# Kernel tuning notes

Measured on AMD Instinct MI355X. Metric: run time of the kernel, lower is better.

The kernel has to match this reference:

```python
import jax, jax.numpy as jnp
import numpy as np

NUM_SUBSET = 3
BN_EPS = 1e-5
T_CONST = 40
NUM_HEADS = 8


def _unit_gcn(x, PA, Wa, ba, Wb, bb, Wd, bd, gamma, beta):
    # x: (B, C, T, V). 1x1 convs become channel einsums. flag=True, GMPool_G,
    # num_point not in {3,7} -> adjacency A = PA only. down = identity (C_in==C_out).
    B, C, T, V = x.shape
    inter = Wa.shape[1]
    x_flat = x.reshape(B, C * T, V)
    y = None
    for i in range(NUM_SUBSET):
        a = jnp.einsum('bctv,ic->bitv', x, Wa[i]) + ba[i][None, :, None, None]
        A1 = a.transpose(0, 3, 1, 2).reshape(B, V, inter * T)          # (B, V, inter*T)
        b = jnp.einsum('bctv,ic->bitv', x, Wb[i]) + bb[i][None, :, None, None]
        A2 = b.reshape(B, inter * T, V)                                 # (B, inter*T, V)
        S = jax.nn.softmax((A1 @ A2) / (inter * T), axis=-2) + PA[i]    # (B, V, V), Softmax(-2)
        z = (x_flat @ S).reshape(B, C, T, V)
        z = jnp.einsum('bctv,oc->botv', z, Wd[i]) + bd[i][None, :, None, None]
        y = z if y is None else y + z
    # BatchNorm2d (eval: running_mean=0, running_var=1)
    y = y * (gamma / jnp.sqrt(1.0 + BN_EPS))[None, :, None, None] + beta[None, :, None, None]
    y = y + x  # residual via identity down-path
    return jax.nn.relu(y)


def _mab_forward(Q, K, fck, fcv, fco):
    B, Npt, DK = K.shape
    T = T_CONST
    C = DK // T
    Kr = K.transpose(0, 2, 1).reshape(B, C, T, Npt)   # (B, C, T, V)
    Kg = _unit_gcn(Kr, *fck)
    Vg = _unit_gcn(Kr, *fcv)
    Kf = Kg.transpose(0, 3, 1, 2).reshape(B, Npt, -1)  # (B, V, C*T)
    Vf = Vg.transpose(0, 3, 1, 2).reshape(B, Npt, -1)
    S, DV = Q.shape[1], Q.shape[2]
    ds = DV // NUM_HEADS
    Qh = Q.reshape(B, S, NUM_HEADS, ds)
    Kh = Kf.reshape(B, Npt, NUM_HEADS, ds)
    Vh = Vf.reshape(B, Npt, NUM_HEADS, ds)
    scores = jnp.einsum('bqhd,bkhd->bhqk', Qh, Kh) / jnp.sqrt(jnp.float32(DV))
    attn = jax.nn.softmax(scores, axis=-1)  # softmax_dim=2 of (H*B, S, V) == last axis
    Oh = Qh + jnp.einsum('bhqk,bkhd->bqhd', attn, Vh)
    O = Oh.reshape(B, S, DV)  # cat over heads along feature dim == reshape
    Og = O.transpose(0, 2, 1).reshape(B, C, T, S)
    Og = _unit_gcn(Og, *fco)
    Og = Og.transpose(0, 3, 1, 2).reshape(B, S, -1)
    return O + jax.nn.relu(Og)


def setup_inputs() -> dict:
    key = jax.random.key(0)
    ks = jax.random.split(key, 8)
    B, Npt, Sd, T, C, inter = 256, 25, 10, 40, 64, 16
    D = C * T  # 2560

    def gcn_params(kk, V):
        k = jax.random.split(kk, 5)
        return dict(
            PA=jnp.full((3, V, V), 1e-6, jnp.float32),
            Wa=jax.random.normal(k[0], (3, inter, C), jnp.float32) * np.float32(np.sqrt(2.0 / C)),
            ba=jnp.zeros((3, inter), jnp.float32),
            Wb=jax.random.normal(k[1], (3, inter, C), jnp.float32) * np.float32(np.sqrt(2.0 / C)),
            bb=jnp.zeros((3, inter), jnp.float32),
            Wd=jax.random.normal(k[2], (3, C, C), jnp.float32) * np.float32(np.sqrt(2.0 / (3 * C))),
            bd=jnp.zeros((3, C), jnp.float32),
            gamma=jax.random.uniform(k[3], (C,), jnp.float32, 0.5, 1.5),
            beta=jax.random.normal(k[4], (C,), jnp.float32) * 0.01,
        )

    inp = {
        'Q': jax.random.normal(ks[0], (B, Sd, D), jnp.float32),
        'K': jax.random.normal(ks[1], (B, Npt, D), jnp.float32),
    }
    for pref, kk, V in (('fck', ks[2], Npt), ('fcv', ks[3], Npt), ('fco', ks[4], Sd)):
        for n, v in gcn_params(kk, V).items():
            inp[pref + '_' + n] = v
    for n in ('relrec_s1', 'relsend_s1', 'relrec_s2', 'relsend_s2', 'relrec_speed', 'relsend_speed'):
        inp[n] = jnp.zeros((1,), jnp.int32)  # unused (branch only active for V==7, T==20)
    return inp


def reference(Q, K,
              fck_PA, fck_Wa, fck_ba, fck_Wb, fck_bb, fck_Wd, fck_bd, fck_gamma, fck_beta,
              fcv_PA, fcv_Wa, fcv_ba, fcv_Wb, fcv_bb, fcv_Wd, fcv_bd, fcv_gamma, fcv_beta,
              fco_PA, fco_Wa, fco_ba, fco_Wb, fco_bb, fco_Wd, fco_bd, fco_gamma, fco_beta,
              relrec_s1, relsend_s1, relrec_s2, relsend_s2, relrec_speed, relsend_speed):
    fck = (fck_PA, fck_Wa, fck_ba, fck_Wb, fck_bb, fck_Wd, fck_bd, fck_gamma, fck_beta)
    fcv = (fcv_PA, fcv_Wa, fcv_ba, fcv_Wb, fcv_bb, fcv_Wd, fcv_bd, fcv_gamma, fcv_beta)
    fco = (fco_PA, fco_Wa, fco_ba, fco_Wb, fco_bb, fco_Wd, fco_bd, fco_gamma, fco_beta)
    return _mab_forward(Q, K, fck, fcv, fco)
```

## Files before the change

kernel.cpp:

```cpp
#include <hip/hip_runtime.h>
#include <hip/hip_bf16.h>

#define BB 256
#define CC 64
#define TT 40
#define DD 2560
#define V1 25
#define V2 10
#define INTER 16
#define NH 8
#define DSH 320
#define HSLAB 8000

typedef __hip_bfloat16 bf16;
typedef unsigned int uint;
typedef unsigned short ushort;
typedef __attribute__((ext_vector_type(8))) short bf16x8;
typedef __attribute__((ext_vector_type(4))) float f32x4;

__device__ __forceinline__ float b2f(bf16 x) { return __bfloat162float(x); }

__device__ __forceinline__ ushort f2bb(float f) {
    uint x = __float_as_uint(f);
    uint r = x + 0x7fffu + ((x >> 16) & 1u);
    return (ushort)(r >> 16);
}
__device__ __forceinline__ float blo(uint u) { return __uint_as_float(u << 16); }
__device__ __forceinline__ float bhi(uint u) { return __uint_as_float(u & 0xffff0000u); }
__device__ __forceinline__ float b2f_us(ushort h) { return __uint_as_float(((uint)h) << 16); }
__device__ __forceinline__ uint4 pack8(const float* a) {
    uint4 pk;
    pk.x = (uint)f2bb(a[0]) | ((uint)f2bb(a[1]) << 16);
    pk.y = (uint)f2bb(a[2]) | ((uint)f2bb(a[3]) << 16);
    pk.z = (uint)f2bb(a[4]) | ((uint)f2bb(a[5]) << 16);
    pk.w = (uint)f2bb(a[6]) | ((uint)f2bb(a[7]) << 16);
    return pk;
}

__device__ __forceinline__ int swz64(int row, int col) {
    return row * 64 + ((((col >> 3) ^ row) & 7) << 3) + (col & 7);
}
__device__ __forceinline__ int swzC(int c, int col) {
    return c * 128 + ((((col >> 3) ^ c) & 15) << 3) + (col & 7);
}

__global__ __launch_bounds__(256) void gcn_S3(
    const float* __restrict__ X,
    const float* __restrict__ Wa0, const float* __restrict__ ba0,
    const float* __restrict__ Wb0, const float* __restrict__ bb0,
    const float* __restrict__ Wa1, const float* __restrict__ ba1,
    const float* __restrict__ Wb1, const float* __restrict__ bb1,
    bf16* __restrict__ Xw, float* __restrict__ Mpart) {
    __shared__ ushort xsT[208][72];
    __shared__ ushort wT[64][72];
    __shared__ ushort abT[4][32][136];
    __shared__ float biasS[64];

    const int tid = threadIdx.x;
    const int b = blockIdx.x & 255, tc = blockIdx.x >> 8;
    const int t0 = tc * 8;
    const int lane = tid & 63, w = tid >> 6;
    const int ln = lane & 15, lq = lane >> 4;

    const float* Xb = X + (size_t)b * V1 * DD;
    for (int e = tid; e < V1 * 64; e += 256) {
        const int v = e >> 6, c = e & 63;
        const float* src = Xb + (size_t)v * DD + c * TT + t0;
        const float4 f0 = *(const float4*)src;
        const float4 f1 = *(const float4*)(src + 4);
        const float tmp[8] = {f0.x, f0.y, f0.z, f0.w, f1.x, f1.y, f1.z, f1.w};
        #pragma unroll
        for (int tl = 0; tl < 8; ++tl) xsT[v * 8 + tl][c] = f2bb(tmp[tl]);
    }
    __syncthreads();

    for (int e = tid; e < 1600; e += 256) {
        const int v = e >> 6, h = (e >> 3) & 7, tl = e & 7;
        *(uint4*)(Xw + (size_t)(b * NH + h) * HSLAB + v * 320 + (t0 + tl) * 8) =
            *(const uint4*)&xsT[v * 8 + tl][h * 8];
    }

    for (int s = 0; s < 3; ++s) {
        if (s) __syncthreads();
        for (int e = tid; e < 4096; e += 256) {
            const int mat = e >> 10, r = e & 1023;
            const float* Wp = (mat == 0) ? Wa0 : (mat == 1) ? Wb0 : (mat == 2) ? Wa1 : Wb1;
            wT[(mat << 4) + (r >> 6)][r & 63] = f2bb(Wp[s * 1024 + r]);
        }
        if (tid < 64) {
            const int mat = tid >> 4, j = tid & 15;
            const float* bp = (mat == 0) ? ba0 : (mat == 1) ? bb0 : (mat == 2) ? ba1 : bb1;
            biasS[tid] = bp[s * 16 + j];
        }
        __syncthreads();

        const bf16x8 a0 = *(const bf16x8*)&wT[w * 16 + ln][lq * 8];
        const bf16x8 a1 = *(const bf16x8*)&wT[w * 16 + ln][lq * 8 + 32];
        float br[4];
        #pragma unroll
        for (int r = 0; r < 4; ++r) br[r] = biasS[w * 16 + lq * 4 + r];
        for (int nt = 0; nt < 13; ++nt) {
            const bf16x8 b0 = *(const bf16x8*)&xsT[nt * 16 + ln][lq * 8];
            const bf16x8 b1 = *(const bf16x8*)&xsT[nt * 16 + ln][lq * 8 + 32];
            f32x4 acc = (f32x4){0.f, 0.f, 0.f, 0.f};
            acc = __builtin_amdgcn_mfma_f32_16x16x32_bf16(a0, b0, acc, 0, 0, 0);
            acc = __builtin_amdgcn_mfma_f32_16x16x32_bf16(a1, b1, acc, 0, 0, 0);
            const int p = nt * 16 + ln;
            if (p < 200) {
                const int v = p >> 3, tl = p & 7;
                #pragma unroll
                for (int r = 0; r < 4; ++r)
                    abT[w][v][(lq * 4 + r) * 8 + tl] = f2bb(acc[r] + br[r]);
            }
        }
        __syncthreads();

        #pragma unroll
        for (int uu = 0; uu < 2; ++uu) {
            const int u = w + uu * 4;
            const int np = u >> 2, mt = (u >> 1) & 1, ntl = u & 1;
            const ushort* Ap = &abT[np * 2 + 0][mt * 16 + ln][lq * 8];
            const ushort* Bp = &abT[np * 2 + 1][ntl * 16 + ln][lq * 8];
            f32x4 g = (f32x4){0.f, 0.f, 0.f, 0.f};
            g = __builtin_amdgcn_mfma_f32_16x16x32_bf16(
                    *(const bf16x8*)Ap, *(const bf16x8*)Bp, g, 0, 0, 0);
            g = __builtin_amdgcn_mfma_f32_16x16x32_bf16(
                    *(const bf16x8*)(Ap + 32), *(const bf16x8*)(Bp + 32), g, 0, 0, 0);
            g = __builtin_amdgcn_mfma_f32_16x16x32_bf16(
                    *(const bf16x8*)(Ap + 64), *(const bf16x8*)(Bp + 64), g, 0, 0, 0);
            g = __builtin_amdgcn_mfma_f32_16x16x32_bf16(
                    *(const bf16x8*)(Ap + 96), *(const bf16x8*)(Bp + 96), g, 0, 0, 0);
            const int vp = ntl * 16 + ln;
            if (vp < V1) {
                float* Mb = Mpart + (((size_t)tc * 256 + b) * 6 + (s * 2 + np)) * 625;
                #pragma unroll
                for (int r = 0; r < 4; ++r) {
                    const int v = mt * 16 + lq * 4 + r;
                    if (v < V1) Mb[v * V1 + vp] = g[r];
                }
            }
        }
    }
}

__global__ __launch_bounds__(128) void reduce_softmax(
    const float* __restrict__ Mpart,
    const float* __restrict__ PA0, const float* __restrict__ PA1,
    const float* __restrict__ WdK, const float* __restrict__ WdV,
    ushort* __restrict__ Sbf, ushort* __restrict__ Wdf) {
    __shared__ float Ms[625];
    const int tid = threadIdx.x, b = blockIdx.x, snp = blockIdx.y;
    const int s = snp >> 1, np = snp & 1;

    if (b == 0) {
        for (int e = tid; e < 256; e += 128) {
            const int wv = e >> 6, l = e & 63;
            const int lnn = l & 15, lqq = l >> 4;
            const float* Wp = (np ? WdV : WdK) + s * 4096 + (wv * 16 + lnn) * 64 + lqq * 8;
            ushort* dst = Wdf + (((np * 3 + s) * 4 + wv) * 64 + l) * 16;
            #pragma unroll
            for (int j = 0; j < 8; ++j) {
                dst[j] = f2bb(Wp[j]);
                dst[8 + j] = f2bb(Wp[32 + j]);
            }
        }
    }

    for (int e = tid; e < 625; e += 128) {
        float sum = 0.f;
        #pragma unroll
        for (int tcc = 0; tcc < 5; ++tcc)
            sum += Mpart[(((size_t)tcc * 256 + b) * 6 + snp) * 625 + e];
        Ms[e] = sum;
    }
    __syncthreads();
    if (tid < 32) {
        ushort* SbfRow = Sbf + ((((size_t)b * 2 + np) * 3 + s) << 10) + tid * 32;
        if (tid < V1) {
            const int vp = tid;
            const float invIT = 1.0f / 640.0f;
            float mx = -1e30f;
            for (int v = 0; v < V1; ++v) mx = fmaxf(mx, Ms[v * V1 + vp]);
            float sum = 0.f;
            for (int v = 0; v < V1; ++v) sum += expf((Ms[v * V1 + vp] - mx) * invIT);
            const float rs = 1.f / sum;
            const float* PAn = np ? PA1 : PA0;
            for (int v = 0; v < V1; ++v) {
                const float e_ = expf((Ms[v * V1 + vp] - mx) * invIT);
                SbfRow[v] = f2bb(e_ * rs + PAn[(s * V1 + v) * V1 + vp]);
            }
            for (int v = V1; v < 32; ++v) SbfRow[v] = 0;
        } else {
            for (int v = 0; v < 32; ++v) SbfRow[v] = 0;
        }
    }
}

__global__ __launch_bounds__(256) void gcn_S2O(
    const float* __restrict__ X,
    const float* __restrict__ Wa0, const float* __restrict__ ba0,
    const float* __restrict__ Wb0, const float* __restrict__ bb0,
    const float* __restrict__ PA0, const float* __restrict__ WdO,
    ushort* __restrict__ SbfO, ushort* __restrict__ Wdf3) {
    constexpr int V = V2;
    constexpr int P = 80;
    __shared__ ushort xs[64][P];
    __shared__ ushort ab[32][P];
    __shared__ ushort wT[64][32];
    __shared__ float biasL[32];
    __shared__ float M[100];

    const int tid = threadIdx.x, b = blockIdx.x, s = blockIdx.y;

    if (b == 0) {
        const int e = tid;
        if (e < 256) {
            const int wv = e >> 6, l = e & 63;
            const int lnn = l & 15, lqq = l >> 4;
            const float* Wp = WdO + s * 4096 + (wv * 16 + lnn) * 64 + lqq * 8;
            ushort* dst = Wdf3 + (((s * 4 + wv) * 64 + l) << 4);
            #pragma unroll
            for (int j = 0; j < 8; ++j) {
                dst[j] = f2bb(Wp[j]);
                dst[8 + j] = f2bb(Wp[32 + j]);
            }
        }
    }

    for (int e = tid; e < 16 * 64; e += 256) {
        int c = e & 63, j = e >> 6;
        wT[c][j]      = f2bb(Wa0[s * 1024 + e]);
        wT[c][16 + j] = f2bb(Wb0[s * 1024 + e]);
    }
    if (tid < 16) {
        biasL[tid]      = ba0[s * 16 + tid];
        biasL[16 + tid] = bb0[s * 16 + tid];
    }

    float macc = 0.f;

    const float* Xb = X + (size_t)b * V * DD;
    for (int tc = 0; tc < 5; ++tc) {
        const int t0 = tc * 8;
        for (int e = tid; e < V * 64; e += 256) {
            const int v = e >> 6, c = e & 63;
            const float* src = Xb + (size_t)v * DD + c * TT + t0;
            const float4 f0 = *(const float4*)src;
            const float4 f1 = *(const float4*)(src + 4);
            const float tmp[8] = {f0.x, f0.y, f0.z, f0.w, f1.x, f1.y, f1.z, f1.w};
            *(uint4*)&xs[c][v * 8] = pack8(tmp);
        }
        __syncthreads();
        for (int tau = tid; tau < 80; tau += 256) {
            const int rq = tau % 8, co = tau / 8;
            float acc[4][8];
            #pragma unroll
            for (int r = 0; r < 4; ++r) {
                const float bv = biasL[4 * rq + r];
                #pragma unroll
                for (int cc = 0; cc < 8; ++cc) acc[r][cc] = bv;
            }
            for (int c = 0; c < 64; ++c) {
                const uint2 wv = *(const uint2*)&wT[c][4 * rq];
                const uint4 xv = *(const uint4*)&xs[c][8 * co];
                const float w0 = blo(wv.x), w1 = bhi(wv.x);
                const float w2 = blo(wv.y), w3 = bhi(wv.y);
                const float x0 = blo(xv.x), x1 = bhi(xv.x);
                const float x2 = blo(xv.y), x3 = bhi(xv.y);
                const float x4 = blo(xv.z), x5 = bhi(xv.z);
                const float x6 = blo(xv.w), x7 = bhi(xv.w);
                acc[0][0] += w0 * x0; acc[0][1] += w0 * x1;
                acc[0][2] += w0 * x2; acc[0][3] += w0 * x3;
                acc[0][4] += w0 * x4; acc[0][5] += w0 * x5;
                acc[0][6] += w0 * x6; acc[0][7] += w0 * x7;
                acc[1][0] += w1 * x0; acc[1][1] += w1 * x1;
                acc[1][2] += w1 * x2; acc[1][3] += w1 * x3;
                acc[1][4] += w1 * x4; acc[1][5] += w1 * x5;
                acc[1][6] += w1 * x6; acc[1][7] += w1 * x7;
                acc[2][0] += w2 * x0; acc[2][1] += w2 * x1;
                acc[2][2] += w2 * x2; acc[2][3] += w2 * x3;
                acc[2][4] += w2 * x4; acc[2][5] += w2 * x5;
                acc[2][6] += w2 * x6; acc[2][7] += w2 * x7;
                acc[3][0] += w3 * x0; acc[3][1] += w3 * x1;
                acc[3][2] += w3 * x2; acc[3][3] += w3 * x3;
                acc[3][4] += w3 * x4; acc[3][5] += w3 * x5;
                acc[3][6] += w3 * x6; acc[3][7] += w3 * x7;
            }
            #pragma unroll
            for (int r = 0; r < 4; ++r)
                *(uint4*)&ab[4 * rq + r][8 * co] = pack8(acc[r]);
        }
        __syncthreads();
        if (tid < 100) {
            const int v = tid / V, vp = tid % V;
            float mm = 0.f;
            #pragma unroll
            for (int j = 0; j < 16; ++j) {
                const uint4 av = *(const uint4*)&ab[j][v * 8];
                const uint4 bv = *(const uint4*)&ab[16 + j][vp * 8];
                mm += blo(av.x) * blo(bv.x) + bhi(av.x) * bhi(bv.x)
                    + blo(av.y) * blo(bv.y) + bhi(av.y) * bhi(bv.y)
                    + blo(av.z) * blo(bv.z) + bhi(av.z) * bhi(bv.z)
                    + blo(av.w) * blo(bv.w) + bhi(av.w) * bhi(bv.w);
            }
            macc += mm;
        }
    }

    if (tid < 100) M[tid] = macc;
    __syncthreads();

    const float invIT = 1.0f / 640.0f;
    if (tid < 16) {
        ushort* So = SbfO + ((size_t)b * 3 + s) * 256 + tid * 16;
        if (tid < V) {
            const int vp = tid;
            float mx = -1e30f;
            for (int v = 0; v < V; ++v) mx = fmaxf(mx, M[v * V + vp]);
            float sum = 0.f;
            for (int v = 0; v < V; ++v) sum += expf((M[v * V + vp] - mx) * invIT);
            const float rs = 1.f / sum;
            for (int v = 0; v < V; ++v) {
                const float e_ = expf((M[v * V + vp] - mx) * invIT);
                So[v] = f2bb(e_ * rs + PA0[(s * V + v) * V + vp]);
            }
            for (int v = V; v < 16; ++v) So[v] = 0;
        } else {
            for (int v = 0; v < 16; ++v) So[v] = 0;
        }
    }
}

__global__ __launch_bounds__(256) void gcn_applyKV(
    const bf16* __restrict__ Xbf,
    const ushort* __restrict__ Sbf, const ushort* __restrict__ Wdf,
    const float* __restrict__ bdK, const float* __restrict__ gK, const float* __restrict__ beK,
    const float* __restrict__ bdV, const float* __restrict__ gV, const float* __restrict__ beV,
    bf16* __restrict__ Kg, bf16* __restrict__ Vg) {

    __shared__ ushort xsT[100 * 64];
    __shared__ ushort SlTs[6144];
    __shared__ ushort uC[8192];
    __shared__ float bias6[6 * 64];

    const int tid = threadIdx.x, b = blockIdx.x, chunk = blockIdx.y;
    const int lane = tid & 63, w = tid >> 6;
    const int ln = lane & 15, lq = lane >> 4;
    const int t0 = chunk * 4;

    if (tid < 64) {
        bias6[tid]       = bdK[tid] + bdK[64 + tid] + bdK[128 + tid];
        bias6[64 + tid]  = bdV[tid] + bdV[64 + tid] + bdV[128 + tid];
        bias6[128 + tid] = gK[tid] * rsqrtf(1.f + 1e-5f);
        bias6[192 + tid] = gV[tid] * rsqrtf(1.f + 1e-5f);
        bias6[256 + tid] = beK[tid];
        bias6[320 + tid] = beV[tid];
    }
    const bf16* Xb = Xbf + (size_t)b * NH * HSLAB;
    for (int e = tid; e < 1024; e += 256) {
        const int h = e >> 7, v = (e >> 2) & 31, tl = e & 3;
        if (v < V1)
            *(uint4*)&xsT[swz64(v * 4 + tl, h * 8)] =
                *(const uint4*)(Xb + (size_t)h * HSLAB + v * 320 + (t0 + tl) * 8);
    }
    {
        const ushort* Sb = Sbf + (size_t)b * 6144;
        for (int e = tid; e < 768; e += 256)
            ((uint4*)SlTs)[e] = ((const uint4*)Sb)[e];
    }
    __syncthreads();

    {
        const int c = lane, q = w;
        #pragma unroll
        for (int j = 0; j < 4; ++j) {
            ushort vals[8];
            #pragma unroll
            for (int i = 0; i < 8; ++i) {
                const int v0 = q * 8 + i;
                vals[i] = (v0 < V1) ? xsT[swz64(v0 * 4 + j, c)] : (ushort)0;
            }
            uint4 pk;
            pk.x = (uint)vals[0] | ((uint)vals[1] << 16);
            pk.y = (uint)vals[2] | ((uint)vals[3] << 16);
            pk.z = (uint)vals[4] | ((uint)vals[5] << 16);
            pk.w = (uint)vals[6] | ((uint)vals[7] << 16);
            *(uint4*)&uC[swzC(c, j * 32 + q * 8)] = pk;
        }
    }
    __syncthreads();

    bf16x8 aF[4];
    #pragma unroll
    for (int tl = 0; tl < 4; ++tl)
        aF[tl] = *(const bf16x8*)&uC[swzC(w * 16 + ln, tl * 32 + lq * 8)];
    __syncthreads();

    for (int g = 0; g < 2; ++g) {
        f32x4 acc[7];
        #pragma unroll
        for (int tn = 0; tn < 7; ++tn) acc[tn] = (f32x4){0.f, 0.f, 0.f, 0.f};

        for (int s = 0; s < 3; ++s) {
            const ushort* wp = Wdf + ((((g * 3 + s) * 4 + w) * 64 + lane) << 4);
            union { uint4 u; bf16x8 v; } ua, ub;
            ua.u = *(const uint4*)wp;
            ub.u = *(const uint4*)(wp + 8);

            if (g | s) __syncthreads();

            #pragma unroll
            for (int nt = 0; nt < 2; ++nt) {
                const bf16x8 bF =
                    *(const bf16x8*)&SlTs[((g * 3 + s) << 10) + (nt * 16 + ln) * 32 + lq * 8];
                const int v = nt * 16 + ln;
                #pragma unroll
                for (int tl = 0; tl < 4; ++tl) {
                    f32x4 d = (f32x4){0.f, 0.f, 0.f, 0.f};
                    d = __builtin_amdgcn_mfma_f32_16x16x32_bf16(aF[tl], bF, d, 0, 0, 0);
                    if (v < V1) {
                        uint2 pk;
                        pk.x = (uint)f2bb(d[0]) | ((uint)f2bb(d[1]) << 16);
                        pk.y = (uint)f2bb(d[2]) | ((uint)f2bb(d[3]) << 16);
                        *(uint2*)&uC[swz64(v * 4 + tl, w * 16 + lq * 4)] = pk;
                    }
                }
            }
            __syncthreads();

            #pragma unroll
            for (int tn = 0; tn < 7; ++tn) {
                const bf16x8 b0 = *(const bf16x8*)&uC[swz64(tn * 16 + ln, lq * 8)];
                const bf16x8 b1 = *(const bf16x8*)&uC[swz64(tn * 16 + ln, lq * 8 + 32)];
                acc[tn] = __builtin_amdgcn_mfma_f32_16x16x32_bf16(ua.v, b0, acc[tn], 0, 0, 0);
                acc[tn] = __builtin_amdgcn_mfma_f32_16x16x32_bf16(ub.v, b1, acc[tn], 0, 0, 0);
            }
        }
        __syncthreads();

        {
            const int c0 = w * 16 + lq * 4;
            float bb[4], ss[4], be[4];
            #pragma unroll
            for (int r = 0; r < 4; ++r) {
                bb[r] = bias6[g * 64 + c0 + r];
                ss[r] = bias6[128 + g * 64 + c0 + r];
                be[r] = bias6[256 + g * 64 + c0 + r];
            }
            #pragma unroll
            for (int tn = 0; tn < 7; ++tn) {
                const int p = tn * 16 + ln;
                if (p < 100) {
                    const uint2 u = *(const uint2*)&xsT[swz64(p, c0)];
                    const float rs[4] = {blo(u.x), bhi(u.x), blo(u.y), bhi(u.y)};
                    float y[4];
                    #pragma unroll
                    for (int r = 0; r < 4; ++r)
                        y[r] = fmaxf((acc[tn][r] + bb[r]) * ss[r] + be[r] + rs[r], 0.f);
                    uint2 pk;
                    pk.x = (uint)f2bb(y[0]) | ((uint)f2bb(y[1]) << 16);
                    pk.y = (uint)f2bb(y[2]) | ((uint)f2bb(y[3]) << 16);
                    *(uint2*)&uC[swz64(p, c0)] = pk;
                }
            }
        }
        __syncthreads();

        bf16* outp = (g ? Vg : Kg) + (size_t)b * NH * HSLAB;
        for (int e = tid; e < 1024; e += 256) {
            const int h = e >> 7, v = (e >> 2) & 31, tl = e & 3;
            if (v < V1)
                *(uint4*)(outp + (size_t)h * HSLAB + v * 320 + (t0 + tl) * 8) =
                    *(const uint4*)&uC[swz64(v * 4 + tl, h * 8)];
        }
    }
}

__global__ __launch_bounds__(256) void gcn_applyO(
    const float* __restrict__ X,
    const ushort* __restrict__ SbfO, const ushort* __restrict__ Wdf3,
    const float* __restrict__ bdO, const float* __restrict__ gO, const float* __restrict__ beO,
    float* __restrict__ out_f, const float* __restrict__ Obuf) {

    __shared__ ushort xsT[80 * 64];
    __shared__ ushort uC[8192];
    __shared__ ushort SlTs16[832];
    __shared__ float bias3[3 * 64];

    const int tid = threadIdx.x, b = blockIdx.x, chunk = blockIdx.y;
    const int lane = tid & 63, w = tid >> 6;
    const int ln = lane & 15, lq = lane >> 4;
    const int t0 = chunk * 8;

    if (tid < 64) {
        bias3[tid]       = bdO[tid] + bdO[64 + tid] + bdO[128 + tid];
        bias3[64 + tid]  = gO[tid] * rsqrtf(1.f + 1e-5f);
        bias3[128 + tid] = beO[tid];
    }
    const float* Xb = X + (size_t)b * V2 * DD;
    for (int e = tid; e < 640; e += 256) {
        const int v = e >> 6, c = e & 63;
        const float* src = Xb + (size_t)v * DD + c * TT + t0;
        const float4 f0 = *(const float4*)src;
        const float4 f1 = *(const float4*)(src + 4);
        const float tmp[8] = {f0.x, f0.y, f0.z, f0.w, f1.x, f1.y, f1.z, f1.w};
        #pragma unroll
        for (int tl = 0; tl < 8; ++tl) xsT[swz64(v * 8 + tl, c)] = f2bb(tmp[tl]);
    }
    {
        const uint4* Sb = (const uint4*)(SbfO + (size_t)b * 768);
        for (int e = tid; e < 96; e += 256) ((uint4*)SlTs16)[e] = Sb[e];
    }
    __syncthreads();

    {
        const int c = lane;
        #pragma unroll
        for (int jj = 0; jj < 4; ++jj) {
            const int u_ = w * 4 + jj;
            const int tl = u_ >> 1, q = u_ & 1;
            ushort vals[8];
            #pragma unroll
            for (int i = 0; i < 8; ++i) {
                const int v0 = q * 8 + i;
                vals[i] = (v0 < V2) ? xsT[swz64(v0 * 8 + tl, c)] : (ushort)0;
            }
            uint4 pk;
            pk.x = (uint)vals[0] | ((uint)vals[1] << 16);
            pk.y = (uint)vals[2] | ((uint)vals[3] << 16);
            pk.z = (uint)vals[4] | ((uint)vals[5] << 16);
            pk.w = (uint)vals[6] | ((uint)vals[7] << 16);
            *(uint4*)&uC[swzC(c, tl * 16 + q * 8)] = pk;
        }
    }
    __syncthreads();

    union { uint4 u; bf16x8 v; } z8; z8.u = (uint4){0u, 0u, 0u, 0u};
    bf16x8 aF[8];
    #pragma unroll
    for (int tl = 0; tl < 8; ++tl)
        aF[tl] = (lq < 2) ? *(const bf16x8*)&uC[swzC(w * 16 + ln, tl * 16 + lq * 8)]
                          : z8.v;
    __syncthreads();

    f32x4 acc[5];
    #pragma unroll
    for (int tn = 0; tn < 5; ++tn) acc[tn] = (f32x4){0.f, 0.f, 0.f, 0.f};

    for (int s = 0; s < 3; ++s) {
        const ushort* wp = Wdf3 + (((s * 4 + w) * 64 + lane) << 4);
        union { uint4 u; bf16x8 v; } ua, ub;
        ua.u = *(const uint4*)wp;
        ub.u = *(const uint4*)(wp + 8);

        if (s) __syncthreads();

        const bf16x8 bF = (lq < 2)
            ? *(const bf16x8*)&SlTs16[s * 256 + ln * 16 + lq * 8] : z8.v;
        #pragma unroll
        for (int tl = 0; tl < 8; ++tl) {
            f32x4 d = (f32x4){0.f, 0.f, 0.f, 0.f};
            d = __builtin_amdgcn_mfma_f32_16x16x32_bf16(aF[tl], bF, d, 0, 0, 0);
            if (ln < V2) {
                uint2 pk;
                pk.x = (uint)f2bb(d[0]) | ((uint)f2bb(d[1]) << 16);
                pk.y = (uint)f2bb(d[2]) | ((uint)f2bb(d[3]) << 16);
                *(uint2*)&uC[swz64(ln * 8 + tl, w * 16 + lq * 4)] = pk;
            }
        }
        __syncthreads();

        #pragma unroll
        for (int tn = 0; tn < 5; ++tn) {
            const bf16x8 b0 = *(const bf16x8*)&uC[swz64(tn * 16 + ln, lq * 8)];
            const bf16x8 b1 = *(const bf16x8*)&uC[swz64(tn * 16 + ln, lq * 8 + 32)];
            acc[tn] = __builtin_amdgcn_mfma_f32_16x16x32_bf16(ua.v, b0, acc[tn], 0, 0, 0);
            acc[tn] = __builtin_amdgcn_mfma_f32_16x16x32_bf16(ub.v, b1, acc[tn], 0, 0, 0);
        }
    }
    __syncthreads();

    {
        const int c0 = w * 16 + lq * 4;
        float bb[4], ss[4], be[4];
        #pragma unroll
        for (int r = 0; r < 4; ++r) {
            bb[r] = bias3[c0 + r];
            ss[r] = bias3[64 + c0 + r];
            be[r] = bias3[128 + c0 + r];
        }
        #pragma unroll
        for (int tn = 0; tn < 5; ++tn) {
            const int p = tn * 16 + ln;
            const uint2 u = *(const uint2*)&xsT[swz64(p, c0)];
            const float rs[4] = {blo(u.x), bhi(u.x), blo(u.y), bhi(u.y)};
            float y[4];
            #pragma unroll
            for (int r = 0; r < 4; ++r)
                y[r] = fmaxf((acc[tn][r] + bb[r]) * ss[r] + be[r] + rs[r], 0.f);
            uint2 pk;
            pk.x = (uint)f2bb(y[0]) | ((uint)f2bb(y[1]) << 16);
            pk.y = (uint)f2bb(y[2]) | ((uint)f2bb(y[3]) << 16);
            *(uint2*)&uC[swz64(p, c0)] = pk;
        }
    }
    __syncthreads();

    {
        const int v = tid & 15, ci = tid >> 4;
        if (v < V2) {
            #pragma unroll
            for (int r = 0; r < 4; ++r) {
                const int c = ci * 4 + r;
                const size_t base = (size_t)b * V2 * DD + (size_t)v * DD + c * TT + t0;
                const float4 o0 = *(const float4*)&Obuf[base];
                const float4 o1 = *(const float4*)&Obuf[base + 4];
                float4 y0, y1;
                y0.x = o0.x + b2f_us(uC[swz64(v * 8 + 0, c)]);
                y0.y = o0.y + b2f_us(uC[swz64(v * 8 + 1, c)]);
                y0.z = o0.z + b2f_us(uC[swz64(v * 8 + 2, c)]);
                y0.w = o0.w + b2f_us(uC[swz64(v * 8 + 3, c)]);
                y1.x = o1.x + b2f_us(uC[swz64(v * 8 + 4, c)]);
                y1.y = o1.y + b2f_us(uC[swz64(v * 8 + 5, c)]);
                y1.z = o1.z + b2f_us(uC[swz64(v * 8 + 6, c)]);
                y1.w = o1.w + b2f_us(uC[swz64(v * 8 + 7, c)]);
                *(float4*)&out_f[base] = y0;
                *(float4*)&out_f[base + 4] = y1;
            }
        }
    }
}

__global__ __launch_bounds__(256) void attn_kernel(const float* __restrict__ Q,
                                                   const bf16* __restrict__ Kg,
                                                   const bf16* __restrict__ Vg,
                                                   float* __restrict__ O) {
    int b = blockIdx.x, h = blockIdx.y, tid = threadIdx.x;
    __shared__ float qs[10 * DSH];
    __shared__ float ks[V1 * 321];
    __shared__ float att[10 * V1];
    const float* Qb = Q + (size_t)b * 10 * DD + h * DSH;
    for (int e = tid; e < 10 * DSH; e += 256) {
        int q = e / DSH, d = e % DSH;
        qs[e] = Qb[(size_t)q * DD + d];
    }
    const bf16* Kb = Kg + (size_t)(b * NH + h) * HSLAB;
    for (int e = tid; e < V1 * TT; e += 256) {
        const int kk = e / TT, t = e % TT;
        const uint4 u = *(const uint4*)(Kb + (size_t)e * 8);
        const ushort* us = (const ushort*)&u;
        float* dst = &ks[kk * 321 + t];
        #pragma unroll
        for (int cl = 0; cl < 8; ++cl) dst[cl * 40] = b2f_us(us[cl]);
    }
    __syncthreads();
    const float scale = 0.019764235376052370f;
    for (int e = tid; e < 10 * V1; e += 256) {
        int q = e / V1, kk = e % V1;
        float acc = 0.f;
        #pragma unroll 8
        for (int d = 0; d < DSH; ++d) acc += qs[q * DSH + d] * ks[kk * 321 + d];
        att[e] = acc * scale;
    }
    __syncthreads();
    if (tid < 10) {
        float mx = -1e30f;
        for (int k = 0; k < V1; ++k) mx = fmaxf(mx, att[tid * V1 + k]);
        float sum = 0.f;
        for (int k = 0; k < V1; ++k) {
            float e_ = expf(att[tid * V1 + k] - mx);
            att[tid * V1 + k] = e_;
            sum += e_;
        }
        float r = 1.0f / sum;
        for (int k = 0; k < V1; ++k) att[tid * V1 + k] *= r;
    }
    const bf16* Vb = Vg + (size_t)(b * NH + h) * HSLAB;
    for (int e = tid; e < V1 * TT; e += 256) {
        const int kk = e / TT, t = e % TT;
        const uint4 u = *(const uint4*)(Vb + (size_t)e * 8);
        const ushort* us = (const ushort*)&u;
        float* dst = &ks[kk * 321 + t];
        #pragma unroll
        for (int cl = 0; cl < 8; ++cl) dst[cl * 40] = b2f_us(us[cl]);
    }
    __syncthreads();
    float* Ob = O + (size_t)b * 10 * DD + h * DSH;
    for (int e = tid; e < 10 * DSH; e += 256) {
        int q = e / DSH, dl = e % DSH;
        float acc = 0.f;
        #pragma unroll
        for (int k = 0; k < V1; ++k) acc += att[q * V1 + k] * ks[k * 321 + dl];
        Ob[(size_t)q * DD + dl] = qs[e] + acc;
    }
}

extern "C" void kernel_launch(void* const* d_in, const int* in_sizes, int n_in,
                              void* d_out, int out_size, void* d_ws, size_t ws_size,
                              hipStream_t stream) {
    const float* Q = (const float*)d_in[0];
    const float* K = (const float*)d_in[1];
    const float* fck_PA = (const float*)d_in[2];
    const float* fck_Wa = (const float*)d_in[3];
    const float* fck_ba = (const float*)d_in[4];
    const float* fck_Wb = (const float*)d_in[5];
    const float* fck_bb = (const float*)d_in[6];
    const float* fck_Wd = (const float*)d_in[7];
    const float* fck_bd = (const float*)d_in[8];
    const float* fck_gamma = (const float*)d_in[9];
    const float* fck_beta = (const float*)d_in[10];
    const float* fcv_PA = (const float*)d_in[11];
    const float* fcv_Wa = (const float*)d_in[12];
    const float* fcv_ba = (const float*)d_in[13];
    const float* fcv_Wb = (const float*)d_in[14];
    const float* fcv_bb = (const float*)d_in[15];
    const float* fcv_Wd = (const float*)d_in[16];
    const float* fcv_bd = (const float*)d_in[17];
    const float* fcv_gamma = (const float*)d_in[18];
    const float* fcv_beta = (const float*)d_in[19];
    const float* fco_PA = (const float*)d_in[20];
    const float* fco_Wa = (const float*)d_in[21];
    const float* fco_ba = (const float*)d_in[22];
    const float* fco_Wb = (const float*)d_in[23];
    const float* fco_bb = (const float*)d_in[24];
    const float* fco_Wd = (const float*)d_in[25];
    const float* fco_bd = (const float*)d_in[26];
    const float* fco_gamma = (const float*)d_in[27];
    const float* fco_beta = (const float*)d_in[28];

    char* wsb = (char*)d_ws;
    bf16* Xbf = (bf16*)(wsb);
    bf16* Vg = (bf16*)(wsb);
    bf16* Kg = (bf16*)(wsb + 32768000);
    float* Mpart = (float*)(wsb + 65536000);
    float* O = (float*)(wsb + 65536000);
    ushort* Sbf = (ushort*)(wsb + 84736000);
    ushort* Wdf = (ushort*)(wsb + 88000000);
    ushort* SbfO = (ushort*)(wsb + 32768000);
    ushort* Wdf3 = (ushort*)(wsb + 33300000);

    gcn_S3<<<dim3(BB * 5), dim3(256), 0, stream>>>(
        K, fck_Wa, fck_ba, fck_Wb, fck_bb,
        fcv_Wa, fcv_ba, fcv_Wb, fcv_bb, Xbf, Mpart);

    reduce_softmax<<<dim3(BB, 6), dim3(128), 0, stream>>>(
        Mpart, fck_PA, fcv_PA, fck_Wd, fcv_Wd, Sbf, Wdf);

    gcn_applyKV<<<dim3(BB, 10), dim3(256), 0, stream>>>(
        Xbf, Sbf, Wdf,
        fck_bd, fck_gamma, fck_beta,
        fcv_bd, fcv_gamma, fcv_beta, Kg, Vg);

    attn_kernel<<<dim3(BB, NH), dim3(256), 0, stream>>>(Q, Kg, Vg, O);

    gcn_S2O<<<dim3(BB, 3), dim3(256), 0, stream>>>(
        O, fco_Wa, fco_ba, fco_Wb, fco_bb, fco_PA, fco_Wd, SbfO, Wdf3);

    gcn_applyO<<<dim3(BB, 5), dim3(256), 0, stream>>>(
        O, SbfO, Wdf3, fco_bd, fco_gamma, fco_beta, (float*)d_out, O);
}
```

Baseline: 466.3 us.

## Pre-pack Wa/Wb weights to bf16 fragments and widen gcn_S3 to 512 threads

```diff
diff --git a/kernel.cpp b/kernel.cpp
--- a/kernel.cpp
+++ b/kernel.cpp
@@ -44,26 +44,44 @@
     return c * 128 + ((((col >> 3) ^ c) & 15) << 3) + (col & 7);
 }
 
-__global__ __launch_bounds__(256) void gcn_S3(
+__global__ __launch_bounds__(256) void prep_wabf(
+    const float* __restrict__ Wa0, const float* __restrict__ Wb0,
+    const float* __restrict__ Wa1, const float* __restrict__ Wb1,
+    ushort* __restrict__ Wabf) {
+    const int tid = threadIdx.x;
+    for (int e = tid; e < 768; e += 256) {
+        const int lane = e & 63, mat = (e >> 6) & 3, s = e >> 8;
+        const int ln = lane & 15, lq = lane >> 4;
+        const float* Wp = (mat == 0) ? Wa0 : (mat == 1) ? Wb0 : (mat == 2) ? Wa1 : Wb1;
+        const float* src = Wp + s * 1024 + ln * 64 + lq * 8;
+        ushort* dst = Wabf + e * 16;
+        #pragma unroll
+        for (int i = 0; i < 8; ++i) {
+            dst[i] = f2bb(src[i]);
+            dst[8 + i] = f2bb(src[32 + i]);
+        }
+    }
+}
+
+__global__ __launch_bounds__(512) void gcn_S3(
     const float* __restrict__ X,
-    const float* __restrict__ Wa0, const float* __restrict__ ba0,
-    const float* __restrict__ Wb0, const float* __restrict__ bb0,
-    const float* __restrict__ Wa1, const float* __restrict__ ba1,
-    const float* __restrict__ Wb1, const float* __restrict__ bb1,
+    const ushort* __restrict__ Wabf,
+    const float* __restrict__ ba0, const float* __restrict__ bb0,
+    const float* __restrict__ ba1, const float* __restrict__ bb1,
     bf16* __restrict__ Xw, float* __restrict__ Mpart) {
     __shared__ ushort xsT[208][72];
-    __shared__ ushort wT[64][72];
     __shared__ ushort abT[4][32][136];
-    __shared__ float biasS[64];
+    __shared__ float biasS3[192];
 
     const int tid = threadIdx.x;
     const int b = blockIdx.x & 255, tc = blockIdx.x >> 8;
     const int t0 = tc * 8;
     const int lane = tid & 63, w = tid >> 6;
     const int ln = lane & 15, lq = lane >> 4;
+    const int mat = w & 3, half = w >> 2;
 
     const float* Xb = X + (size_t)b * V1 * DD;
-    for (int e = tid; e < V1 * 64; e += 256) {
+    for (int e = tid; e < V1 * 64; e += 512) {
         const int v = e >> 6, c = e & 63;
         const float* src = Xb + (size_t)v * DD + c * TT + t0;
         const float4 f0 = *(const float4*)src;
@@ -72,53 +90,49 @@
         #pragma unroll
         for (int tl = 0; tl < 8; ++tl) xsT[v * 8 + tl][c] = f2bb(tmp[tl]);
     }
-    __syncthreads();
-
-    for (int e = tid; e < 1600; e += 256) {
+    if (tid < 192) {
+        const int s = tid >> 6, m2 = (tid >> 4) & 3, j = tid & 15;
+        const float* bp = (m2 == 0) ? ba0 : (m2 == 1) ? bb0 : (m2 == 2) ? ba1 : bb1;
+        biasS3[tid] = bp[s * 16 + j];
+    }
+    __syncthreads();
+
+    for (int e = tid; e < 1600; e += 512) {
         const int v = e >> 6, h = (e >> 3) & 7, tl = e & 7;
         *(uint4*)(Xw + (size_t)(b * NH + h) * HSLAB + v * 320 + (t0 + tl) * 8) =
             *(const uint4*)&xsT[v * 8 + tl][h * 8];
     }
 
     for (int s = 0; s < 3; ++s) {
+        const ushort* wp = Wabf + (((s * 4 + mat) * 64 + lane) << 4);
+        union { uint4 u; bf16x8 v; } ua, ub;
+        ua.u = *(const uint4*)wp;
+        ub.u = *(const uint4*)(wp + 8);
+        float br[4];
+        #pragma unroll
+        for (int r = 0; r < 4; ++r) br[r] = biasS3[s * 64 + mat * 16 + lq * 4 + r];
+
         if (s) __syncthreads();
-        for (int e = tid; e < 4096; e += 256) {
-            const int mat = e >> 10, r = e & 1023;
-            const float* Wp = (mat == 0) ? Wa0 : (mat == 1) ? Wb0 : (mat == 2) ? Wa1 : Wb1;
-            wT[(mat << 4) + (r >> 6)][r & 63] = f2bb(Wp[s * 1024 + r]);
-        }
-        if (tid < 64) {
-            const int mat = tid >> 4, j = tid & 15;
-            const float* bp = (mat == 0) ? ba0 : (mat == 1) ? bb0 : (mat == 2) ? ba1 : bb1;
-            biasS[tid] = bp[s * 16 + j];
-        }
-        __syncthreads();
-
-        const bf16x8 a0 = *(const bf16x8*)&wT[w * 16 + ln][lq * 8];
-        const bf16x8 a1 = *(const bf16x8*)&wT[w * 16 + ln][lq * 8 + 32];
-        float br[4];
-        #pragma unroll
-        for (int r = 0; r < 4; ++r) br[r] = biasS[w * 16 + lq * 4 + r];
-        for (int nt = 0; nt < 13; ++nt) {
+
+        const int ntEnd = half ? 13 : 7;
+        for (int nt = half ? 7 : 0; nt < ntEnd; ++nt) {
             const bf16x8 b0 = *(const bf16x8*)&xsT[nt * 16 + ln][lq * 8];
             const bf16x8 b1 = *(const bf16x8*)&xsT[nt * 16 + ln][lq * 8 + 32];
             f32x4 acc = (f32x4){0.f, 0.f, 0.f, 0.f};
-            acc = __builtin_amdgcn_mfma_f32_16x16x32_bf16(a0, b0, acc, 0, 0, 0);
-            acc = __builtin_amdgcn_mfma_f32_16x16x32_bf16(a1, b1, acc, 0, 0, 0);
+            acc = __builtin_amdgcn_mfma_f32_16x16x32_bf16(ua.v, b0, acc, 0, 0, 0);
+            acc = __builtin_amdgcn_mfma_f32_16x16x32_bf16(ub.v, b1, acc, 0, 0, 0);
             const int p = nt * 16 + ln;
             if (p < 200) {
                 const int v = p >> 3, tl = p & 7;
                 #pragma unroll
                 for (int r = 0; r < 4; ++r)
-                    abT[w][v][(lq * 4 + r) * 8 + tl] = f2bb(acc[r] + br[r]);
+                    abT[mat][v][(lq * 4 + r) * 8 + tl] = f2bb(acc[r] + br[r]);
             }
         }
         __syncthreads();
 
-        #pragma unroll
-        for (int uu = 0; uu < 2; ++uu) {
-            const int u = w + uu * 4;
-            const int np = u >> 2, mt = (u >> 1) & 1, ntl = u & 1;
+        {
+            const int np = w >> 2, mt = (w >> 1) & 1, ntl = w & 1;
             const ushort* Ap = &abT[np * 2 + 0][mt * 16 + ln][lq * 8];
             const ushort* Bp = &abT[np * 2 + 1][ntl * 16 + ln][lq * 8];
             f32x4 g = (f32x4){0.f, 0.f, 0.f, 0.f};
@@ -738,10 +752,13 @@
     ushort* Wdf = (ushort*)(wsb + 88000000);
     ushort* SbfO = (ushort*)(wsb + 32768000);
     ushort* Wdf3 = (ushort*)(wsb + 33300000);
-
-    gcn_S3<<<dim3(BB * 5), dim3(256), 0, stream>>>(
-        K, fck_Wa, fck_ba, fck_Wb, fck_bb,
-        fcv_Wa, fcv_ba, fcv_Wb, fcv_bb, Xbf, Mpart);
+    ushort* Wabf = (ushort*)(wsb + 95590400);
+
+    prep_wabf<<<dim3(1), dim3(256), 0, stream>>>(
+        fck_Wa, fck_Wb, fcv_Wa, fcv_Wb, Wabf);
+
+    gcn_S3<<<dim3(BB * 5), dim3(512), 0, stream>>>(
+        K, Wabf, fck_ba, fck_bb, fcv_ba, fcv_bb, Xbf, Mpart);
 
     reduce_softmax<<<dim3(BB, 6), dim3(128), 0, stream>>>(
         Mpart, fck_PA, fcv_PA, fck_Wd, fcv_Wd, Sbf, Wdf);
```

After: 446.4 us. 4.3% less time.
